# Kernel tuning notes

Hardware: AMD Instinct MI355X
Metric: run time of the kernel (lower is better)

The kernel has to match this reference:

```python
import jax, jax.numpy as jnp
import numpy as np

T, B, D, H, L = 1024, 64, 512, 512, 2


def setup_inputs() -> dict:
    key = jax.random.key(0)
    ks = jax.random.split(key, 10)
    s = 1.0 / np.sqrt(D)
    return {
        "x": jax.random.normal(ks[0], (T, B, D), jnp.float32),
        "hidden": jax.random.normal(ks[1], (L, B, H), jnp.float32),
        "fc_w": jax.random.normal(ks[2], (D, D), jnp.float32) * s,
        "fc_b": jax.random.normal(ks[3], (D,), jnp.float32) * s,
        "w0": jax.random.normal(ks[4], (H, D), jnp.float32) * s,
        "b0": jax.random.normal(ks[5], (H,), jnp.float32) * s,
        "u0": jax.random.uniform(ks[6], (H,), jnp.float32, -1.0, 1.0),
        "w1": jax.random.normal(ks[7], (H, H), jnp.float32) * s,
        "b1": jax.random.normal(ks[8], (H,), jnp.float32) * s,
        "u1": jax.random.uniform(ks[9], (H,), jnp.float32, -1.0, 1.0),
    }


def _indrnn_layer(inp, h0, w, b, u):
    # Precompute input projection for all timesteps: [T, B, H]
    pre = jnp.einsum("tbd,hd->tbh", inp, w) + b

    def step(h, p):
        h_new = jax.nn.relu(p + u * h)  # elementwise recurrent weight
        return h_new, h_new

    h_last, outs = jax.lax.scan(step, h0, pre)
    return outs, h_last


def reference(x, hidden, fc_w, fc_b, w0, b0, u0, w1, b1, u1):
    # fc layer before the IndRNN stack
    x = jnp.einsum("tbd,ed->tbe", x, fc_w) + fc_b
    out0, h0 = _indrnn_layer(x, hidden[0], w0, b0, u0)
    out1, h1 = _indrnn_layer(out0, hidden[1], w1, b1, u1)
    hn = jnp.stack([h0, h1], axis=0)  # [L, B, H]
    return out1, hn
```

## Files before the change

kernel.cpp:

```cpp
#include <hip/hip_runtime.h>
#include <hip/hip_bf16.h>
#include <cstdint>
#include <cstddef>

#define T_DIM 1024
#define B_DIM 64
#define D_DIM 512
#define H_DIM 512
#define TBROWS (T_DIM * B_DIM)
#define BH (B_DIM * H_DIM)
#define TBH ((size_t)T_DIM * (size_t)BH)

typedef __bf16 bf16x8 __attribute__((ext_vector_type(8)));
typedef float floatx4 __attribute__((ext_vector_type(4)));

__device__ __forceinline__ void async_load16(const void* g, void* l) {
  __builtin_amdgcn_global_load_lds(
      (const __attribute__((address_space(1))) unsigned int*)g,
      (__attribute__((address_space(3))) unsigned int*)l,
      16, 0, 0);
}

__device__ __forceinline__ void wait_vm(int n) {
  switch (n) {
    case 4:  asm volatile("s_waitcnt vmcnt(4)"  ::: "memory"); break;
    case 8:  asm volatile("s_waitcnt vmcnt(8)"  ::: "memory"); break;
    case 12: asm volatile("s_waitcnt vmcnt(12)" ::: "memory"); break;
    case 16: asm volatile("s_waitcnt vmcnt(16)" ::: "memory"); break;
    case 24: asm volatile("s_waitcnt vmcnt(24)" ::: "memory"); break;
    case 32: asm volatile("s_waitcnt vmcnt(32)" ::: "memory"); break;
    case 40: asm volatile("s_waitcnt vmcnt(40)" ::: "memory"); break;
    case 48: asm volatile("s_waitcnt vmcnt(48)" ::: "memory"); break;
    default: asm volatile("s_waitcnt vmcnt(0)"  ::: "memory"); break;
  }
}

__device__ __forceinline__ int xcd_swizzle(int bid, int nwg) {
  return (bid & 7) * (nwg >> 3) + (bid >> 3);
}

__global__ __launch_bounds__(256) void prep_kernel(
    const float* __restrict__ w0, const float* __restrict__ fc_w,
    const float* __restrict__ fc_b, const float* __restrict__ b0,
    const float* __restrict__ w1, __bf16* __restrict__ Wc,
    __bf16* __restrict__ w1bf, float* __restrict__ bcomb) {
  const int blk = blockIdx.x;
  const int tid = threadIdx.x;
  if (blk < 128) {
    const int h0 = (blk >> 1) * 8;
    const int d = ((blk & 1) << 8) + tid;
    float a[8];
#pragma unroll
    for (int j = 0; j < 8; j++) a[j] = 0.f;
#pragma unroll 4
    for (int e = 0; e < D_DIM; ++e) {
      const float fv = fc_w[(size_t)e * D_DIM + d];
#pragma unroll
      for (int j = 0; j < 8; j++)
        a[j] = fmaf(w0[(size_t)(h0 + j) * D_DIM + e], fv, a[j]);
    }
#pragma unroll
    for (int j = 0; j < 8; j++)
      Wc[(size_t)(h0 + j) * D_DIM + d] = (__bf16)a[j];
  } else if (blk < 256) {
    const long i = ((long)(blk - 128) * 256 + tid) * 8;
    const float4 a = *(const float4*)(w1 + i);
    const float4 b = *(const float4*)(w1 + i + 4);
    bf16x8 v;
    v[0] = (__bf16)a.x; v[1] = (__bf16)a.y; v[2] = (__bf16)a.z; v[3] = (__bf16)a.w;
    v[4] = (__bf16)b.x; v[5] = (__bf16)b.y; v[6] = (__bf16)b.z; v[7] = (__bf16)b.w;
    *(bf16x8*)(w1bf + i) = v;
  } else {
    const int h = (blk - 256) * 256 + tid;
    float acc = b0[h];
    const float4* w4 = (const float4*)(w0 + (size_t)h * D_DIM);
#pragma unroll 4
    for (int e = 0; e < D_DIM / 4; ++e) {
      const float4 wv = w4[e];
      acc = fmaf(wv.x, fc_b[e * 4 + 0], acc);
      acc = fmaf(wv.y, fc_b[e * 4 + 1], acc);
      acc = fmaf(wv.z, fc_b[e * 4 + 2], acc);
      acc = fmaf(wv.w, fc_b[e * 4 + 3], acc);
    }
    bcomb[h] = acc;
  }
}

__global__ __launch_bounds__(512, 1) void gemm_a32_4ph(
    const float* __restrict__ A,
    const __bf16* __restrict__ Bm,
    const float* __restrict__ bias,
    __bf16* __restrict__ C,
    int M, int N, int K) {
  __shared__ float Asf[2][2][128 * 32];
  __shared__ __bf16 Bs[2][2][256 * 32];

  const int tid = threadIdx.x;
  const int lane = tid & 63;
  const int wave = tid >> 6;
  const int wg = xcd_swizzle((int)blockIdx.x, (int)gridDim.x);
  const int nb = N / 256;
  const int bm = wg / nb;
  const int bn = wg % nb;
  const int m0 = bm * 128, n0 = bn * 256;

  floatx4 zero = {0.f, 0.f, 0.f, 0.f};
  floatx4 acc[4][4];
#pragma unroll
  for (int i = 0; i < 4; i++)
#pragma unroll
    for (int j = 0; j < 4; j++) acc[i][j] = zero;

  const int tm = (wave >> 2) * 64;
  const int tn = (wave & 3) * 64;
  const int lrow = lane & 15;
  const int lk = (lane >> 4) * 8;
  const int sB = lane >> 4;
  const int s0 = lk >> 2;

  auto S = [&](int t, int c) {
    const int p = t & 1;
    const int k0 = t * 64 + c * 32;
#pragma unroll
    for (int i = 0; i < 2; i++) {
      const int u = wave * 2 + i;
      {
        const int e = u * 64 + lane;
        const int r = e >> 3;
        const int g = (e & 7) ^ (r & 7);
        async_load16(&A[(size_t)(m0 + r) * K + k0 + g * 4],
                     &Asf[p][c][u * 256]);
      }
      {
        const int e = u * 64 + lane;
        const int r = e >> 2;
        const int g = (e & 3) ^ ((r >> 1) & 3);
        async_load16(&Bm[(size_t)(n0 + r) * K + k0 + g * 8],
                     &Bs[p][c][u * 512]);
      }
    }
  };

  S(0, 0); S(0, 1); S(1, 0); S(1, 1);

  const int F = (K >> 6) << 1;
  for (int f = 0; f < F; ++f) {
    const int t = f >> 1, c = f & 1, p = t & 1;
    if (f >= 1 && f + 3 < F) S((f + 3) >> 1, (f + 3) & 1);

    const int rem = F - 1 - f;
    wait_vm(rem >= 3 ? 12 : rem * 4);
    __builtin_amdgcn_s_barrier();
    __builtin_amdgcn_sched_barrier(0);

    bf16x8 af[4], bfr[4];
#pragma unroll
    for (int i = 0; i < 4; i++) {
      const int ra = tm + i * 16 + lrow;
      const int k7 = ra & 7;
      const float4 fa = *(const float4*)&Asf[p][c][ra * 32 + ((s0 ^ k7) << 2)];
      const float4 fb = *(const float4*)&Asf[p][c][ra * 32 + (((s0 + 1) ^ k7) << 2)];
      bf16x8 v;
      v[0] = (__bf16)fa.x; v[1] = (__bf16)fa.y; v[2] = (__bf16)fa.z; v[3] = (__bf16)fa.w;
      v[4] = (__bf16)fb.x; v[5] = (__bf16)fb.y; v[6] = (__bf16)fb.z; v[7] = (__bf16)fb.w;
      af[i] = v;
      const int rb = tn + i * 16 + lrow;
      bfr[i] = *(const bf16x8*)&Bs[p][c][rb * 32 + ((sB ^ ((rb >> 1) & 3)) << 3)];
    }
    __builtin_amdgcn_s_setprio(1);
#pragma unroll
    for (int i = 0; i < 4; i++)
#pragma unroll
      for (int j = 0; j < 4; j++)
        acc[i][j] = __builtin_amdgcn_mfma_f32_16x16x32_bf16(af[i], bfr[j],
                                                            acc[i][j], 0, 0, 0);
    __builtin_amdgcn_s_setprio(0);
    __builtin_amdgcn_sched_barrier(0);
    __builtin_amdgcn_s_barrier();
    __builtin_amdgcn_sched_barrier(0);
  }

  const int ccol = lane & 15;
  const int crow = (lane >> 4) * 4;
  float bv[4];
#pragma unroll
  for (int j = 0; j < 4; j++) bv[j] = bias[n0 + tn + j * 16 + ccol];
#pragma unroll
  for (int i = 0; i < 4; i++) {
#pragma unroll
    for (int j = 0; j < 4; j++) {
      const size_t base =
          (size_t)(m0 + tm + i * 16 + crow) * N + (n0 + tn + j * 16 + ccol);
#pragma unroll
      for (int r = 0; r < 4; r++)
        C[base + (size_t)r * N] = (__bf16)(acc[i][j][r] + bv[j]);
    }
  }
}

__global__ __launch_bounds__(512, 1) void gemm_bt_bias_8ph(
    const __bf16* __restrict__ A,
    const __bf16* __restrict__ Bm,
    const float* __restrict__ bias,
    __bf16* __restrict__ C,
    int M, int N, int K) {
  __shared__ __bf16 As[2][2][256 * 32];
  __shared__ __bf16 Bs[2][2][256 * 32];

  const int tid = threadIdx.x;
  const int lane = tid & 63;
  const int wave = tid >> 6;
  const int wg = xcd_swizzle((int)blockIdx.x, (int)gridDim.x);
  const int nb = N / 256;
  const int bm = wg / nb;
  const int bn = wg % nb;
  const int m0 = bm * 256, n0 = bn * 256;

  floatx4 zero = {0.f, 0.f, 0.f, 0.f};
  floatx4 acc[8][4];
#pragma unroll
  for (int i = 0; i < 8; i++)
#pragma unroll
    for (int j = 0; j < 4; j++) acc[i][j] = zero;

  const int tm = (wave >> 2) * 128;
  const int tn = (wave & 3) * 64;
  const int lrow = lane & 15;
  const int sB = lane >> 4;

  auto S = [&](int t, int c) {
    const int p = t & 1;
    const int k0 = t * 64 + c * 32;
#pragma unroll
    for (int i = 0; i < 2; i++) {
      const int u = wave * 2 + i;
      const int e = u * 64 + lane;
      const int r = e >> 2;
      const int g = (e & 3) ^ ((r >> 1) & 3);
      async_load16(&A[(size_t)(m0 + r) * K + k0 + g * 8], &As[p][c][u * 512]);
      async_load16(&Bm[(size_t)(n0 + r) * K + k0 + g * 8], &Bs[p][c][u * 512]);
    }
  };

  S(0, 0); S(0, 1); S(1, 0); S(1, 1);

  const int F = (K >> 6) << 1;
  for (int f = 0; f < F; ++f) {
    const int t = f >> 1, c = f & 1, p = t & 1;
    if (f >= 1 && f + 3 < F) S((f + 3) >> 1, (f + 3) & 1);

    const int rem = F - 1 - f;
    wait_vm(rem >= 3 ? 12 : rem * 4);
    __builtin_amdgcn_s_barrier();
    __builtin_amdgcn_sched_barrier(0);

    bf16x8 af[8], bfr[4];
#pragma unroll
    for (int i = 0; i < 8; i++) {
      const int ra = tm + i * 16 + lrow;
      af[i] = *(const bf16x8*)&As[p][c][ra * 32 + ((sB ^ ((ra >> 1) & 3)) << 3)];
    }
#pragma unroll
    for (int j = 0; j < 4; j++) {
      const int rb = tn + j * 16 + lrow;
      bfr[j] = *(const bf16x8*)&Bs[p][c][rb * 32 + ((sB ^ ((rb >> 1) & 3)) << 3)];
    }
    __builtin_amdgcn_s_setprio(1);
#pragma unroll
    for (int i = 0; i < 8; i++)
#pragma unroll
      for (int j = 0; j < 4; j++)
        acc[i][j] = __builtin_amdgcn_mfma_f32_16x16x32_bf16(af[i], bfr[j],
                                                            acc[i][j], 0, 0, 0);
    __builtin_amdgcn_s_setprio(0);
    __builtin_amdgcn_sched_barrier(0);
    __builtin_amdgcn_s_barrier();
    __builtin_amdgcn_sched_barrier(0);
  }

  const int ccol = lane & 15;
  const int crow = (lane >> 4) * 4;
  float bv[4];
#pragma unroll
  for (int j = 0; j < 4; j++) bv[j] = bias[n0 + tn + j * 16 + ccol];
#pragma unroll
  for (int i = 0; i < 8; i++) {
#pragma unroll
    for (int j = 0; j < 4; j++) {
      const size_t base =
          (size_t)(m0 + tm + i * 16 + crow) * N + (n0 + tn + j * 16 + ccol);
#pragma unroll
      for (int r = 0; r < 4; r++)
        C[base + (size_t)r * N] = (__bf16)(acc[i][j][r] + bv[j]);
    }
  }
}

#define TS 64
#define NTILE (T_DIM / TS)

template <bool BF16OUT>
__global__ __launch_bounds__(64, 1) void scan_kernel(
    const __bf16* __restrict__ pre,
    const float* __restrict__ h0,
    const float* __restrict__ u,
    void* __restrict__ outp,
    float* __restrict__ hn) {
  constexpr int OBYTES = BF16OUT ? 2 : 4;
  __shared__ __bf16 tin[3][TS * 64];
  __shared__ char oraw[2][TS * 64 * OBYTES];

  const int lane = threadIdx.x;
  const int c0 = blockIdx.x * 64;
  const int idx = c0 + lane;
  const float uu = u[idx & (H_DIM - 1)];
  float h = h0[idx];

  const int lrow = lane >> 3;
  const int lcg = (lane & 7) * 8;

#pragma unroll
  for (int i = 0; i < 8; i++)
    async_load16(&pre[(size_t)(i * 8 + lrow) * BH + c0 + lcg], &tin[0][i * 512]);
#pragma unroll
  for (int i = 0; i < 8; i++)
    async_load16(&pre[(size_t)(TS + i * 8 + lrow) * BH + c0 + lcg],
                 &tin[1][i * 512]);

  for (int tile = 0; tile < NTILE; ++tile) {
    __builtin_amdgcn_sched_barrier(0);
    if (tile + 2 < NTILE) {
      const int nb = (tile + 2) % 3;
      const size_t nt0 = (size_t)(tile + 2) * TS;
#pragma unroll
      for (int i = 0; i < 8; i++)
        async_load16(&pre[(nt0 + i * 8 + lrow) * BH + c0 + lcg],
                     &tin[nb][i * 512]);
    }
    int wv;
    if (BF16OUT)
      wv = (tile == 0 || tile == NTILE - 1) ? 16
         : (tile == 1 || tile == NTILE - 2) ? 24 : 32;
    else
      wv = (tile == 0) ? 16
         : (tile == 1 || tile == NTILE - 1) ? 32
         : (tile == NTILE - 2) ? 40 : 48;
    wait_vm(wv);
    __builtin_amdgcn_sched_barrier(0);

    const int buf = tile % 3;
    const int t0 = tile * TS;
    char* ob = oraw[tile & 1];
#pragma unroll
    for (int s = 0; s < TS; s++) {
      const float p = (float)tin[buf][s * 64 + lane];
      h = fmaxf(fmaf(uu, h, p), 0.0f);
      if (BF16OUT) ((__bf16*)ob)[s * 64 + lane] = (__bf16)h;
      else         ((float*)ob)[s * 64 + lane] = h;
    }
    if (BF16OUT) {
#pragma unroll
      for (int i = 0; i < 8; i++) {
        const int row = i * 8 + (lane >> 3);
        const bf16x8 v =
            *(const bf16x8*)&((const __bf16*)ob)[row * 64 + (lane & 7) * 8];
        *(bf16x8*)&((__bf16*)outp)[(size_t)(t0 + row) * BH + c0 + (lane & 7) * 8] = v;
      }
    } else {
#pragma unroll
      for (int i = 0; i < 16; i++) {
        const int row = i * 4 + (lane >> 4);
        const float4 v =
            *(const float4*)&((const float*)ob)[row * 64 + (lane & 15) * 4];
        *(float4*)&((float*)outp)[(size_t)(t0 + row) * BH + c0 + (lane & 15) * 4] = v;
      }
    }
  }
  hn[idx] = h;
}

extern "C" void kernel_launch(void* const* d_in, const int* in_sizes, int n_in,
                              void* d_out, int out_size, void* d_ws,
                              size_t ws_size, hipStream_t stream) {
  (void)in_sizes; (void)n_in; (void)out_size; (void)ws_size;
  const float* x      = (const float*)d_in[0];
  const float* hidden = (const float*)d_in[1];
  const float* fc_w   = (const float*)d_in[2];
  const float* fc_b   = (const float*)d_in[3];
  const float* w0     = (const float*)d_in[4];
  const float* b0     = (const float*)d_in[5];
  const float* u0     = (const float*)d_in[6];
  const float* w1     = (const float*)d_in[7];
  const float* b1     = (const float*)d_in[8];
  const float* u1     = (const float*)d_in[9];
  float* out = (float*)d_out;

  char* ws = (char*)d_ws;
  __bf16* pre  = (__bf16*)ws;
  __bf16* out0 = (__bf16*)(ws + TBH * 2);
  char*   tail = ws + 2 * TBH * 2;
  __bf16* Wc    = (__bf16*)tail;
  __bf16* w1bf  = (__bf16*)(tail + 512 * 1024);
  float*  bcomb = (float*)(tail + 1024 * 1024);

  float* hn = out + TBH;

  prep_kernel<<<258, 256, 0, stream>>>(w0, fc_w, fc_b, b0, w1, Wc, w1bf, bcomb);
  gemm_a32_4ph<<<(TBROWS / 128) * (H_DIM / 256), 512, 0, stream>>>(
      x, Wc, bcomb, pre, TBROWS, H_DIM, D_DIM);
  scan_kernel<true><<<BH / 64, 64, 0, stream>>>(pre, hidden, u0, (void*)out0, hn);
  gemm_bt_bias_8ph<<<(TBROWS / 256) * (H_DIM / 256), 512, 0, stream>>>(
      out0, w1bf, b1, pre, TBROWS, H_DIM, H_DIM);
  scan_kernel<false><<<BH / 64, 64, 0, stream>>>(pre, hidden + BH, u1,
                                                 (void*)out, hn + BH);
}
```

Measured before the change: 490.4 us.

## Enlarge fc-fused GEMM tile to 256x256 with three-stage LDS ring

The fp32-input projection GEMM now computes 256x256 output tiles per block instead of 128x256, with each wave owning 128x64. The K pipeline becomes a three-buffer ring of 32-wide slices, and each prefetch is issued after the consuming barrier instead of a 2x2 phase double buffer. This increases operand reuse per LDS load and per block, and halves the grid. The cost is more accumulator registers and LDS, and fewer blocks to spread across CUs.

```diff
diff --git a/kernel.cpp b/kernel.cpp
--- a/kernel.cpp
+++ b/kernel.cpp
@@ -24,6 +24,7 @@
 __device__ __forceinline__ void wait_vm(int n) {
   switch (n) {
     case 4:  asm volatile("s_waitcnt vmcnt(4)"  ::: "memory"); break;
+    case 6:  asm volatile("s_waitcnt vmcnt(6)"  ::: "memory"); break;
     case 8:  asm volatile("s_waitcnt vmcnt(8)"  ::: "memory"); break;
     case 12: asm volatile("s_waitcnt vmcnt(12)" ::: "memory"); break;
     case 16: asm volatile("s_waitcnt vmcnt(16)" ::: "memory"); break;
@@ -86,14 +87,14 @@
   }
 }
 
-__global__ __launch_bounds__(512, 1) void gemm_a32_4ph(
+__global__ __launch_bounds__(512, 1) void gemm_a32_r3(
     const float* __restrict__ A,
     const __bf16* __restrict__ Bm,
     const float* __restrict__ bias,
     __bf16* __restrict__ C,
     int M, int N, int K) {
-  __shared__ float Asf[2][2][128 * 32];
-  __shared__ __bf16 Bs[2][2][256 * 32];
+  __shared__ float Asf[3][256 * 32];
+  __shared__ __bf16 Bs[3][256 * 32];
 
   const int tid = threadIdx.x;
   const int lane = tid & 63;
@@ -102,74 +103,72 @@
   const int nb = N / 256;
   const int bm = wg / nb;
   const int bn = wg % nb;
-  const int m0 = bm * 128, n0 = bn * 256;
+  const int m0 = bm * 256, n0 = bn * 256;
 
   floatx4 zero = {0.f, 0.f, 0.f, 0.f};
-  floatx4 acc[4][4];
-#pragma unroll
-  for (int i = 0; i < 4; i++)
+  floatx4 acc[8][4];
+#pragma unroll
+  for (int i = 0; i < 8; i++)
 #pragma unroll
     for (int j = 0; j < 4; j++) acc[i][j] = zero;
 
-  const int tm = (wave >> 2) * 64;
+  const int tm = (wave >> 2) * 128;
   const int tn = (wave & 3) * 64;
   const int lrow = lane & 15;
   const int lk = (lane >> 4) * 8;
   const int sB = lane >> 4;
   const int s0 = lk >> 2;
 
-  auto S = [&](int t, int c) {
-    const int p = t & 1;
-    const int k0 = t * 64 + c * 32;
+  auto S = [&](int t, int pl) {
+    const int k0 = t * 32;
+#pragma unroll
+    for (int i = 0; i < 4; i++) {
+      const int u = wave * 4 + i;
+      const int e = u * 64 + lane;
+      const int r = e >> 3;
+      const int g = (e & 7) ^ (r & 7);
+      async_load16(&A[(size_t)(m0 + r) * K + k0 + g * 4], &Asf[pl][u * 256]);
+    }
 #pragma unroll
     for (int i = 0; i < 2; i++) {
       const int u = wave * 2 + i;
-      {
-        const int e = u * 64 + lane;
-        const int r = e >> 3;
-        const int g = (e & 7) ^ (r & 7);
-        async_load16(&A[(size_t)(m0 + r) * K + k0 + g * 4],
-                     &Asf[p][c][u * 256]);
-      }
-      {
-        const int e = u * 64 + lane;
-        const int r = e >> 2;
-        const int g = (e & 3) ^ ((r >> 1) & 3);
-        async_load16(&Bm[(size_t)(n0 + r) * K + k0 + g * 8],
-                     &Bs[p][c][u * 512]);
-      }
+      const int e = u * 64 + lane;
+      const int r = e >> 2;
+      const int g = (e & 3) ^ ((r >> 1) & 3);
+      async_load16(&Bm[(size_t)(n0 + r) * K + k0 + g * 8], &Bs[pl][u * 512]);
     }
   };
 
-  S(0, 0); S(0, 1); S(1, 0); S(1, 1);
-
-  const int F = (K >> 6) << 1;
+  S(0, 0); S(1, 1); S(2, 2);
+
+  const int F = K / 32;
   for (int f = 0; f < F; ++f) {
-    const int t = f >> 1, c = f & 1, p = t & 1;
-    if (f >= 1 && f + 3 < F) S((f + 3) >> 1, (f + 3) & 1);
-
+    const int pl = f % 3;
     const int rem = F - 1 - f;
-    wait_vm(rem >= 3 ? 12 : rem * 4);
+    wait_vm(rem >= 2 ? 12 : (rem == 1 ? 6 : 0));
     __builtin_amdgcn_s_barrier();
     __builtin_amdgcn_sched_barrier(0);
 
-    bf16x8 af[4], bfr[4];
-#pragma unroll
-    for (int i = 0; i < 4; i++) {
+    bf16x8 af[8], bfr[4];
+#pragma unroll
+    for (int i = 0; i < 8; i++) {
       const int ra = tm + i * 16 + lrow;
       const int k7 = ra & 7;
-      const float4 fa = *(const float4*)&Asf[p][c][ra * 32 + ((s0 ^ k7) << 2)];
-      const float4 fb = *(const float4*)&Asf[p][c][ra * 32 + (((s0 + 1) ^ k7) << 2)];
+      const float4 fa = *(const float4*)&Asf[pl][ra * 32 + ((s0 ^ k7) << 2)];
+      const float4 fb = *(const float4*)&Asf[pl][ra * 32 + (((s0 + 1) ^ k7) << 2)];
       bf16x8 v;
       v[0] = (__bf16)fa.x; v[1] = (__bf16)fa.y; v[2] = (__bf16)fa.z; v[3] = (__bf16)fa.w;
       v[4] = (__bf16)fb.x; v[5] = (__bf16)fb.y; v[6] = (__bf16)fb.z; v[7] = (__bf16)fb.w;
       af[i] = v;
-      const int rb = tn + i * 16 + lrow;
-      bfr[i] = *(const bf16x8*)&Bs[p][c][rb * 32 + ((sB ^ ((rb >> 1) & 3)) << 3)];
+    }
+#pragma unroll
+    for (int j = 0; j < 4; j++) {
+      const int rb = tn + j * 16 + lrow;
+      bfr[j] = *(const bf16x8*)&Bs[pl][rb * 32 + ((sB ^ ((rb >> 1) & 3)) << 3)];
     }
     __builtin_amdgcn_s_setprio(1);
 #pragma unroll
-    for (int i = 0; i < 4; i++)
+    for (int i = 0; i < 8; i++)
 #pragma unroll
       for (int j = 0; j < 4; j++)
         acc[i][j] = __builtin_amdgcn_mfma_f32_16x16x32_bf16(af[i], bfr[j],
@@ -178,6 +177,7 @@
     __builtin_amdgcn_sched_barrier(0);
     __builtin_amdgcn_s_barrier();
     __builtin_amdgcn_sched_barrier(0);
+    if (f + 3 < F) S(f + 3, pl);
   }
 
   const int ccol = lane & 15;
@@ -186,7 +186,7 @@
 #pragma unroll
   for (int j = 0; j < 4; j++) bv[j] = bias[n0 + tn + j * 16 + ccol];
 #pragma unroll
-  for (int i = 0; i < 4; i++) {
+  for (int i = 0; i < 8; i++) {
 #pragma unroll
     for (int j = 0; j < 4; j++) {
       const size_t base =
@@ -406,7 +406,7 @@
   float* hn = out + TBH;
 
   prep_kernel<<<258, 256, 0, stream>>>(w0, fc_w, fc_b, b0, w1, Wc, w1bf, bcomb);
-  gemm_a32_4ph<<<(TBROWS / 128) * (H_DIM / 256), 512, 0, stream>>>(
+  gemm_a32_r3<<<(TBROWS / 256) * (H_DIM / 256), 512, 0, stream>>>(
       x, Wc, bcomb, pre, TBROWS, H_DIM, D_DIM);
   scan_kernel<true><<<BH / 64, 64, 0, stream>>>(pre, hidden, u0, (void*)out0, hn);
   gemm_bt_bias_8ph<<<(TBROWS / 256) * (H_DIM / 256), 512, 0, stream>>>(
```

After: 449.7 us. 8.3% less time.

## Convert fp32 A tile to bf16 in registers before LDS in first GEMM

Applied to the files above, without the earlier changes.

The first GEMM now loads fp32 A rows into registers, converts them to bf16 and writes bf16 tiles into a 4-slot LDS ring. B still streams in asynchronously via global_load_lds. The kernel moves to 1024-thread blocks computing 256x256 tiles with K fixed at 512, replacing the per-wave fp32-to-bf16 conversion at fragment-read time. The goal is to halve LDS footprint and read traffic for A and deepen the pipeline, at the cost of register staging, hard-coded K, and more complex vmcnt bookkeeping.

```diff
diff --git a/kernel.cpp b/kernel.cpp
--- a/kernel.cpp
+++ b/kernel.cpp
@@ -23,8 +23,12 @@
 
 __device__ __forceinline__ void wait_vm(int n) {
   switch (n) {
+    case 2:  asm volatile("s_waitcnt vmcnt(2)"  ::: "memory"); break;
     case 4:  asm volatile("s_waitcnt vmcnt(4)"  ::: "memory"); break;
+    case 5:  asm volatile("s_waitcnt vmcnt(5)"  ::: "memory"); break;
+    case 6:  asm volatile("s_waitcnt vmcnt(6)"  ::: "memory"); break;
     case 8:  asm volatile("s_waitcnt vmcnt(8)"  ::: "memory"); break;
+    case 9:  asm volatile("s_waitcnt vmcnt(9)"  ::: "memory"); break;
     case 12: asm volatile("s_waitcnt vmcnt(12)" ::: "memory"); break;
     case 16: asm volatile("s_waitcnt vmcnt(16)" ::: "memory"); break;
     case 24: asm volatile("s_waitcnt vmcnt(24)" ::: "memory"); break;
@@ -86,14 +90,17 @@
   }
 }
 
-__global__ __launch_bounds__(512, 1) void gemm_a32_4ph(
+__global__ __launch_bounds__(1024, 1) void gemm_a32_rs(
     const float* __restrict__ A,
     const __bf16* __restrict__ Bm,
     const float* __restrict__ bias,
     __bf16* __restrict__ C,
-    int M, int N, int K) {
-  __shared__ float Asf[2][2][128 * 32];
-  __shared__ __bf16 Bs[2][2][256 * 32];
+    int M, int N, int Kdummy) {
+  (void)Kdummy;
+  constexpr int K = 512;
+  constexpr int F = K / 32;
+  __shared__ __bf16 As[4][256 * 32];
+  __shared__ __bf16 Bs[4][256 * 32];
 
   const int tid = threadIdx.x;
   const int lane = tid & 63;
@@ -102,7 +109,7 @@
   const int nb = N / 256;
   const int bm = wg / nb;
   const int bn = wg % nb;
-  const int m0 = bm * 128, n0 = bn * 256;
+  const int m0 = bm * 256, n0 = bn * 256;
 
   floatx4 zero = {0.f, 0.f, 0.f, 0.f};
   floatx4 acc[4][4];
@@ -114,58 +121,62 @@
   const int tm = (wave >> 2) * 64;
   const int tn = (wave & 3) * 64;
   const int lrow = lane & 15;
-  const int lk = (lane >> 4) * 8;
   const int sB = lane >> 4;
-  const int s0 = lk >> 2;
-
-  auto S = [&](int t, int c) {
-    const int p = t & 1;
-    const int k0 = t * 64 + c * 32;
-#pragma unroll
-    for (int i = 0; i < 2; i++) {
-      const int u = wave * 2 + i;
-      {
-        const int e = u * 64 + lane;
-        const int r = e >> 3;
-        const int g = (e & 7) ^ (r & 7);
-        async_load16(&A[(size_t)(m0 + r) * K + k0 + g * 4],
-                     &Asf[p][c][u * 256]);
-      }
-      {
-        const int e = u * 64 + lane;
-        const int r = e >> 2;
-        const int g = (e & 3) ^ ((r >> 1) & 3);
-        async_load16(&Bm[(size_t)(n0 + r) * K + k0 + g * 8],
-                     &Bs[p][c][u * 512]);
-      }
-    }
+
+  const int arow = wave * 16 + (lane >> 2);
+  const int ap = lane & 3;
+  const int ag = ap ^ ((arow >> 1) & 3);
+  const float* Aw = A + (size_t)(m0 + arow) * K + ag * 8;
+
+  const int br = wave * 16 + (lane >> 2);
+  const int bg = (lane & 3) ^ ((br >> 1) & 3);
+  const __bf16* Bw = Bm + (size_t)(n0 + br) * K + bg * 8;
+
+  float4 rA0[2], rA1[2];
+
+  auto loadA = [&](float4* s, int p) {
+    const float* gp = Aw + p * 32;
+    s[0] = *(const float4*)(gp);
+    s[1] = *(const float4*)(gp + 4);
   };
-
-  S(0, 0); S(0, 1); S(1, 0); S(1, 1);
-
-  const int F = (K >> 6) << 1;
-  for (int f = 0; f < F; ++f) {
-    const int t = f >> 1, c = f & 1, p = t & 1;
-    if (f >= 1 && f + 3 < F) S((f + 3) >> 1, (f + 3) & 1);
-
-    const int rem = F - 1 - f;
-    wait_vm(rem >= 3 ? 12 : rem * 4);
+  auto writeA = [&](float4* s, int p) {
+    bf16x8 v;
+    v[0] = (__bf16)s[0].x; v[1] = (__bf16)s[0].y;
+    v[2] = (__bf16)s[0].z; v[3] = (__bf16)s[0].w;
+    v[4] = (__bf16)s[1].x; v[5] = (__bf16)s[1].y;
+    v[6] = (__bf16)s[1].z; v[7] = (__bf16)s[1].w;
+    *(bf16x8*)&As[p & 3][arow * 32 + ap * 8] = v;
+  };
+  auto issueB = [&](int p) {
+    async_load16(Bw + (size_t)p * 32, &Bs[p & 3][wave * 512]);
+  };
+  auto kc = [&](int g) { return g <= F - 4 ? 3 : (g == F - 3 ? 2 : 0); };
+
+  issueB(0);
+  loadA(rA0, 0); issueB(1);
+  loadA(rA1, 1); issueB(2);
+  writeA(rA0, 0);
+  asm volatile("s_waitcnt lgkmcnt(0)" ::: "memory");
+  __builtin_amdgcn_sched_barrier(0);
+
+  auto phase = [&](int f, float4* Ls, float4* Ws) {
+    __builtin_amdgcn_sched_barrier(0);
+    if (f + 2 < F) loadA(Ls, f + 2);
+    if (f + 3 < F) issueB(f + 3);
+    __builtin_amdgcn_sched_barrier(0);
+    wait_vm(kc(f - 2) + kc(f - 1) + kc(f));
+    __builtin_amdgcn_sched_barrier(0);
     __builtin_amdgcn_s_barrier();
     __builtin_amdgcn_sched_barrier(0);
 
+    const int sl = f & 3;
     bf16x8 af[4], bfr[4];
 #pragma unroll
     for (int i = 0; i < 4; i++) {
       const int ra = tm + i * 16 + lrow;
-      const int k7 = ra & 7;
-      const float4 fa = *(const float4*)&Asf[p][c][ra * 32 + ((s0 ^ k7) << 2)];
-      const float4 fb = *(const float4*)&Asf[p][c][ra * 32 + (((s0 + 1) ^ k7) << 2)];
-      bf16x8 v;
-      v[0] = (__bf16)fa.x; v[1] = (__bf16)fa.y; v[2] = (__bf16)fa.z; v[3] = (__bf16)fa.w;
-      v[4] = (__bf16)fb.x; v[5] = (__bf16)fb.y; v[6] = (__bf16)fb.z; v[7] = (__bf16)fb.w;
-      af[i] = v;
+      af[i] = *(const bf16x8*)&As[sl][ra * 32 + ((sB ^ ((ra >> 1) & 3)) << 3)];
       const int rb = tn + i * 16 + lrow;
-      bfr[i] = *(const bf16x8*)&Bs[p][c][rb * 32 + ((sB ^ ((rb >> 1) & 3)) << 3)];
+      bfr[i] = *(const bf16x8*)&Bs[sl][rb * 32 + ((sB ^ ((rb >> 1) & 3)) << 3)];
     }
     __builtin_amdgcn_s_setprio(1);
 #pragma unroll
@@ -176,8 +187,17 @@
                                                             acc[i][j], 0, 0, 0);
     __builtin_amdgcn_s_setprio(0);
     __builtin_amdgcn_sched_barrier(0);
+    if (f + 1 < F) writeA(Ws, f + 1);
+    asm volatile("s_waitcnt lgkmcnt(0)" ::: "memory");
+    __builtin_amdgcn_sched_barrier(0);
     __builtin_amdgcn_s_barrier();
     __builtin_amdgcn_sched_barrier(0);
+  };
+
+#pragma unroll
+  for (int ff = 0; ff < F; ff += 2) {
+    phase(ff + 0, rA0, rA1);
+    phase(ff + 1, rA1, rA0);
   }
 
   const int ccol = lane & 15;
@@ -406,7 +426,7 @@
   float* hn = out + TBH;
 
   prep_kernel<<<258, 256, 0, stream>>>(w0, fc_w, fc_b, b0, w1, Wc, w1bf, bcomb);
-  gemm_a32_4ph<<<(TBROWS / 128) * (H_DIM / 256), 512, 0, stream>>>(
+  gemm_a32_rs<<<(TBROWS / 256) * (H_DIM / 256), 1024, 0, stream>>>(
       x, Wc, bcomb, pre, TBROWS, H_DIM, D_DIM);
   scan_kernel<true><<<BH / 64, 64, 0, stream>>>(pre, hidden, u0, (void*)out0, hn);
   gemm_bt_bias_8ph<<<(TBROWS / 256) * (H_DIM / 256), 512, 0, stream>>>(
```

New measurement: 460.6 us. -6.1%, faster.
